# Kernel optimization log

Hardware: AMD Instinct MI355X
Metric: run time of the kernel (lower is better)

## Reference

```python
import jax, jax.numpy as jnp
import numpy as np

B, S, D, H = 2, 2048, 2048, 16
HD = D // H                     # head_dim = 128
ROTARY_BASE = 10000.0
CAP = 50.0                      # self.cap = FloatTensor([50.0])
FMIN = float(np.finfo(np.float32).min)
SCALE = 1.0 / np.sqrt(HD).astype(np.float32)


def _rope_sincos(seq_len, dim):
    # fixed_pos_embedding_factory with scaling_factor=1, no expand
    inv_freq = 1.0 / ROTARY_BASE ** (2.0 * jnp.arange(dim // 2, dtype=jnp.float32) / dim)
    pos = jnp.arange(seq_len, dtype=jnp.float32)
    ang = pos[:, None] * inv_freq[None, :]          # [S, dim/2]
    return jnp.sin(ang), jnp.cos(ang)


def _apply_rotary(x, sin, cos):
    # x: [B,S,H,hd]; sin/cos: [S,hd/2]. duplicate_interleave is a no-op
    # (view(-1,1).repeat(1,1).view(dim0,-1) returns m unchanged), so this is
    # NeoX-style (split-half) rotary.
    sin = sin[None, :, None, :]
    cos = cos[None, :, None, :]
    x1, x2 = jnp.split(x, 2, axis=-1)
    return jnp.concatenate([x1 * cos - x2 * sin, x2 * cos + x1 * sin], axis=-1)


def setup_inputs() -> dict:
    key = jax.random.key(0)
    kx, kq, kk, kv, ko = jax.random.split(key, 5)
    w = 0.02
    return {
        "x":  jax.random.normal(kx, (B, S, D), jnp.float32),
        "Wq": jax.random.normal(kq, (D, D), jnp.float32) * w,
        "Wk": jax.random.normal(kk, (D, D), jnp.float32) * w,
        "Wv": jax.random.normal(kv, (D, D), jnp.float32) * w,
        "Wo": jax.random.normal(ko, (D, D), jnp.float32) * w,
    }


def reference(x, Wq, Wk, Wv, Wo):
    # projections (bias=False)
    q = (x @ Wq).reshape(B, S, H, HD)
    k = (x @ Wk).reshape(B, S, H, HD)
    v = (x @ Wv).reshape(B, S, H, HD)

    # rotary over the full head dim (rotary_pct = 1.0)
    sin, cos = _rope_sincos(S, HD)
    q = _apply_rotary(q, sin, cos)
    k = _apply_rotary(k, sin, cos)

    # [B,H,S,hd]
    q = q.transpose(0, 2, 1, 3)
    k = k.transpose(0, 2, 1, 3)
    v = v.transpose(0, 2, 1, 3)

    # scores [B,H,S,S]
    scores = jnp.einsum("bhqd,bhkd->bhqk", q, k) * SCALE

    # logit cap: cap * tanh(x / cap)
    scores = CAP * jnp.tanh(scores / CAP)

    # causal mask (tril bias buffer), masked to finfo.min
    causal = jnp.tril(jnp.ones((S, S), dtype=bool))
    scores = jnp.where(causal[None, None], scores, FMIN)

    # LingvoSoftmax: softmax with an extra zero logit appended per row
    m = jnp.maximum(jnp.max(scores, axis=-1, keepdims=True), 0.0)
    e = jnp.exp(scores - m)
    denom = jnp.sum(e, axis=-1, keepdims=True) + jnp.exp(-m)
    probs = e / denom

    out = jnp.einsum("bhqk,bhkd->bhqd", probs, v)      # [B,H,S,hd]
    out = out.transpose(0, 2, 1, 3).reshape(B, S, D)
    return out @ Wo
```

## Files before the change

kernel.cpp:

```cpp
#include <hip/hip_runtime.h>
#include <hip/hip_bf16.h>

#define B_  2
#define S_  2048
#define D_  2048
#define H_  16
#define HD_ 128

typedef unsigned short u16;
typedef __attribute__((ext_vector_type(8))) short bf16x8;
typedef __attribute__((ext_vector_type(4))) float f32x4;
typedef __attribute__((ext_vector_type(16))) float f32x16;

#define GLOAD_LDS16(g, l)                                                     \
  __builtin_amdgcn_global_load_lds(                                           \
      (const __attribute__((address_space(1))) void*)(g),                     \
      (__attribute__((address_space(3))) void*)(l), 16, 0, 0)

__device__ __forceinline__ u16 f2bf(float f){
  unsigned u; __builtin_memcpy(&u, &f, 4);
  u += 0x7fffu + ((u >> 16) & 1u);
  return (u16)(u >> 16);
}
__device__ __forceinline__ float bf2f(u16 h){
  unsigned u = ((unsigned)h) << 16; float f; __builtin_memcpy(&f, &u, 4); return f;
}
__device__ __forceinline__ unsigned pack_bf16x2(float lo, float hi){
  __hip_bfloat162 h2 = __float22bfloat162_rn(float2{lo, hi});
  unsigned u; __builtin_memcpy(&u, &h2, 4); return u;
}

__global__ void cast_x_kernel(const float* __restrict__ x, u16* __restrict__ xb){
  int i = blockIdx.x * 256 + threadIdx.x;
  float4 v = reinterpret_cast<const float4*>(x)[i];
  ushort4 o; o.x = f2bf(v.x); o.y = f2bf(v.y); o.z = f2bf(v.z); o.w = f2bf(v.w);
  reinterpret_cast<ushort4*>(xb)[i] = o;
}

__global__ void wtrans_kernel(const float* __restrict__ w0, const float* __restrict__ w1,
                              const float* __restrict__ w2, const float* __restrict__ w3,
                              u16* __restrict__ o0, u16* __restrict__ o1,
                              u16* __restrict__ o2, u16* __restrict__ o3){
  __shared__ float t[32][33];
  const float* src; u16* dst;
  switch (blockIdx.z){
    case 0:  src = w0; dst = o0; break;
    case 1:  src = w1; dst = o1; break;
    case 2:  src = w2; dst = o2; break;
    default: src = w3; dst = o3; break;
  }
  int j0 = blockIdx.x * 32, i0 = blockIdx.y * 32;
  int tx = threadIdx.x & 31, ty = threadIdx.x >> 5;
  #pragma unroll
  for (int rr = 0; rr < 4; ++rr)
    t[ty + rr*8][tx] = src[(size_t)(i0 + ty + rr*8) * D_ + j0 + tx];
  __syncthreads();
  #pragma unroll
  for (int rr = 0; rr < 4; ++rr)
    dst[(size_t)(j0 + ty + rr*8) * D_ + i0 + tx] = f2bf(t[tx][ty + rr*8]);
}

template<int MODE>
__global__ __launch_bounds__(256) void gemm128_kernel(
    const u16* __restrict__ A,
    const u16* __restrict__ B0, const u16* __restrict__ B1, const u16* __restrict__ B2,
    u16* __restrict__ qb, u16* __restrict__ kb, u16* __restrict__ vtb,
    float* __restrict__ outp)
{
  constexpr int K = 2048;
  __shared__ u16 As[128 * 32];
  __shared__ u16 Bs[128 * 32];
  const int bid = blockIdx.x;
  const int xcd = bid & 7, loc = bid >> 3;
  const int mq  = loc & 31;
  const int nl  = loc >> 5;
  const int by  = (MODE == 0) ? (xcd * 6 + nl) : (xcd * 2 + nl);
  const int m0  = mq * 128;
  int which, n0;
  const u16* Bmat;
  if (MODE == 0){ which = by >> 4; n0 = (by & 15) * 128;
                  Bmat = (which == 0) ? B0 : ((which == 1) ? B1 : B2); }
  else          { which = 0; n0 = by * 128; Bmat = B0; }

  int tid  = threadIdx.x;
  int lane = tid & 63;
  int wid  = tid >> 6;
  int wr = wid >> 1, wc = wid & 1;
  int g = lane >> 4, r = lane & 15;

  f32x4 zero = {0.f, 0.f, 0.f, 0.f};
  f32x4 acc[4][4];
  #pragma unroll
  for (int i = 0; i < 4; ++i)
    #pragma unroll
    for (int j = 0; j < 4; ++j) acc[i][j] = zero;

  for (int kt = 0; kt < K; kt += 32){
    #pragma unroll
    for (int jj = 0; jj < 2; ++jj){
      int cbase = wid * 64 + jj * 256;
      int c  = cbase + lane;
      int rr = c >> 2, c8 = c & 3;
      GLOAD_LDS16(&A[(size_t)(m0 + rr) * K + kt + c8 * 8],    &As[cbase * 8]);
      GLOAD_LDS16(&Bmat[(size_t)(n0 + rr) * K + kt + c8 * 8], &Bs[cbase * 8]);
    }
    asm volatile("s_waitcnt vmcnt(0)" ::: "memory");
    __syncthreads();
    bf16x8 af[4], bfr[4];
    #pragma unroll
    for (int i = 0; i < 4; ++i)
      af[i]  = *reinterpret_cast<bf16x8*>(&As[(wr*64 + i*16 + r) * 32 + g * 8]);
    #pragma unroll
    for (int i = 0; i < 4; ++i)
      bfr[i] = *reinterpret_cast<bf16x8*>(&Bs[(wc*64 + i*16 + r) * 32 + g * 8]);
    #pragma unroll
    for (int i = 0; i < 4; ++i)
      #pragma unroll
      for (int j = 0; j < 4; ++j)
        acc[i][j] = __builtin_amdgcn_mfma_f32_16x16x32_bf16(af[i], bfr[j], acc[i][j], 0, 0, 0);
    __syncthreads();
  }

  #pragma unroll
  for (int i = 0; i < 4; ++i){
    int row0 = m0 + wr*64 + i*16 + g*4;
    int b  = row0 >> 11, s0 = row0 & (S_ - 1);
    #pragma unroll
    for (int j = 0; j < 4; ++j){
      int col = n0 + wc*64 + j*16 + r;
      if (MODE == 1){
        #pragma unroll
        for (int e = 0; e < 4; ++e)
          outp[(size_t)(row0 + e) * D_ + col] = acc[i][j][e];
      } else {
        int h = col >> 7, d = col & 127;
        int bh = b * H_ + h;
        if (which == 2){
          ushort4 pk;
          pk.x = f2bf(acc[i][j][0]); pk.y = f2bf(acc[i][j][1]);
          pk.z = f2bf(acc[i][j][2]); pk.w = f2bf(acc[i][j][3]);
          *reinterpret_cast<ushort4*>(&vtb[((size_t)bh * HD_ + d) * S_ + s0]) = pk;
        } else {
          u16* dstb = (which == 0) ? qb : kb;
          #pragma unroll
          for (int e = 0; e < 4; ++e)
            dstb[((size_t)bh * S_ + s0 + e) * HD_ + d] = f2bf(acc[i][j][e]);
        }
      }
    }
  }
}

__global__ void rope_kernel(u16* __restrict__ qbuf, u16* __restrict__ kbuf){
  int idx = blockIdx.x * 256 + threadIdx.x;
  int j  = idx & 63;
  int s  = (idx >> 6) & (S_ - 1);
  int bh = idx >> 17;
  const float LOG2_1E4 = 13.287712379549449f;
  float inv = exp2f(-(float)(2 * j) * (LOG2_1E4 / 128.f));
  float ang = (float)s * inv;
  float sn = __sinf(ang), cs = __cosf(ang);
  size_t base = ((size_t)bh * S_ + s) * HD_;
  float x1 = bf2f(qbuf[base + j]), x2 = bf2f(qbuf[base + 64 + j]);
  qbuf[base + j]      = f2bf(x1 * cs - x2 * sn);
  qbuf[base + 64 + j] = f2bf(x2 * cs + x1 * sn);
  float y1 = bf2f(kbuf[base + j]), y2 = bf2f(kbuf[base + 64 + j]);
  kbuf[base + j]      = f2bf(y1 * cs - y2 * sn);
  kbuf[base + 64 + j] = f2bf(y2 * cs + y1 * sn);
}

__global__ __launch_bounds__(256) void attn6_kernel(
  const u16* __restrict__ qbuf, const u16* __restrict__ kbuf,
  const u16* __restrict__ vtb,  u16* __restrict__ ob)
{
  __shared__ u16 Klds[2][64 * 128];
  __shared__ u16 Vlds[2][128 * 64];

  const int lane = threadIdx.x & 63;
  const int wid  = threadIdx.x >> 6;
  const int r    = lane & 31;
  const int hi   = lane >> 5;
  const int bh   = blockIdx.x;
  const int qblk = 15 - blockIdx.y;
  const int qc   = qblk * 128 + wid * 32;
  const int qc32 = qc >> 5;
  const int T    = 2 * qblk + 2;

  const float SCALE = 0.08838834764831845f;

  const size_t sbase = (size_t)bh * S_ * HD_;
  const size_t vbase = (size_t)bh * HD_ * S_;

  bf16x8 qf[8];
  {
    const u16* qrow = qbuf + sbase + (size_t)(qc + r) * HD_ + hi * 8;
    #pragma unroll
    for (int cc = 0; cc < 8; ++cc)
      qf[cc] = *reinterpret_cast<const bf16x8*>(qrow + cc * 16);
  }

  f32x16 oacc[4];
  #pragma unroll
  for (int i = 0; i < 4; ++i)
    #pragma unroll
    for (int j = 0; j < 16; ++j) oacc[i][j] = 0.f;
  float lsum = 0.f;

  auto stage = [&](int buf, int t){
    const int kv0 = t * 64;
    u16* Kt = &Klds[buf][0];
    u16* Vt = &Vlds[buf][0];
    #pragma unroll
    for (int j = 0; j < 4; ++j){
      const int cbase = j * 256 + wid * 64;
      const int ck = cbase + lane;
      const int krow = ck >> 4, kslot = ck & 15;
      GLOAD_LDS16(kbuf + sbase + (size_t)(kv0 + krow) * HD_ + ((kslot ^ (krow & 15)) * 8),
                  Kt + cbase * 8);
      const int vd = ck >> 3, vslot = ck & 7;
      GLOAD_LDS16(vtb + vbase + (size_t)vd * S_ + kv0 + ((vslot ^ (vd & 7)) * 8),
                  Vt + cbase * 8);
    }
  };

  stage(0, 0);
  asm volatile("s_waitcnt vmcnt(0)" ::: "memory");
  __syncthreads();

  for (int t = 0; t < T; ++t){
    const int cur = t & 1;
    if (t + 1 < T) stage(cur ^ 1, t + 1);

    const u16* Kt = &Klds[cur][0];
    const u16* Vt = &Vlds[cur][0];
    #pragma unroll
    for (int sub = 0; sub < 2; ++sub){
      const int t32 = 2 * t + sub;
      if (t32 <= qc32){
        const bool diag = (t32 == qc32);
        f32x16 sc;
        #pragma unroll
        for (int j = 0; j < 16; ++j) sc[j] = 0.f;
        #pragma unroll
        for (int cc = 0; cc < 8; ++cc){
          const int row = sub * 32 + r;
          const int slot = (cc * 2 + hi) ^ (r & 15);
          bf16x8 kf = *reinterpret_cast<const bf16x8*>(&Kt[row * 128 + slot * 8]);
          sc = __builtin_amdgcn_mfma_f32_32x32x16_bf16(kf, qf[cc], sc, 0, 0, 0);
        }
        float p[16];
        #pragma unroll
        for (int reg = 0; reg < 16; ++reg){
          float tt = sc[reg] * SCALE;
          float u  = tt * tt * 4.0e-4f;
          float capped = tt * (1.f - u * 0.33333333f + u * u * 0.13333333f);
          float pv = __expf(capped);
          if (diag){
            int kl = (reg & 3) + 8 * (reg >> 2) + 4 * hi;
            if (kl > r) pv = 0.f;
          }
          p[reg] = pv;
          lsum += pv;
        }
        unsigned a[4], b[4];
        #pragma unroll
        for (int r4 = 0; r4 < 4; ++r4){
          a[r4] = pack_bf16x2(p[r4*4+0], p[r4*4+1]);
          b[r4] = pack_bf16x2(p[r4*4+2], p[r4*4+3]);
        }
        unsigned ra0 = __shfl_xor(hi ? a[0] : a[1], 32);
        unsigned rb0 = __shfl_xor(hi ? b[0] : b[1], 32);
        unsigned ra1 = __shfl_xor(hi ? a[2] : a[3], 32);
        unsigned rb1 = __shfl_xor(hi ? b[2] : b[3], 32);
        unsigned pw[8];
        pw[0] = hi ? ra0 : a[0];  pw[1] = hi ? rb0 : b[0];
        pw[2] = hi ? a[1] : ra0;  pw[3] = hi ? b[1] : rb0;
        pw[4] = hi ? ra1 : a[2];  pw[5] = hi ? rb1 : b[2];
        pw[6] = hi ? a[3] : ra1;  pw[7] = hi ? b[3] : rb1;
        bf16x8 pb0, pb1;
        __builtin_memcpy(&pb0, &pw[0], 16);
        __builtin_memcpy(&pb1, &pw[4], 16);
        #pragma unroll
        for (int i = 0; i < 4; ++i){
          const int d  = i * 32 + r;
          const int sw = d & 7;
          bf16x8 vf0 = *reinterpret_cast<const bf16x8*>(
              &Vt[d * 64 + (((sub * 4 + hi) ^ sw) * 8)]);
          oacc[i] = __builtin_amdgcn_mfma_f32_32x32x16_bf16(vf0, pb0, oacc[i], 0, 0, 0);
          bf16x8 vf1 = *reinterpret_cast<const bf16x8*>(
              &Vt[d * 64 + (((sub * 4 + 2 + hi) ^ sw) * 8)]);
          oacc[i] = __builtin_amdgcn_mfma_f32_32x32x16_bf16(vf1, pb1, oacc[i], 0, 0, 0);
        }
      }
    }
    asm volatile("s_waitcnt vmcnt(0)" ::: "memory");
    __syncthreads();
  }

  float lt = lsum + __shfl_xor(lsum, 32);
  float linv = 1.0f / (1.0f + lt);

  const int b = bh >> 4, h = bh & 15;
  u16* orow = ob + ((size_t)(b * S_ + qc + r)) * D_ + h * HD_;
  #pragma unroll
  for (int i = 0; i < 4; ++i){
    #pragma unroll
    for (int r4 = 0; r4 < 4; ++r4){
      ushort4 st;
      st.x = f2bf(oacc[i][r4*4+0] * linv);
      st.y = f2bf(oacc[i][r4*4+1] * linv);
      st.z = f2bf(oacc[i][r4*4+2] * linv);
      st.w = f2bf(oacc[i][r4*4+3] * linv);
      *reinterpret_cast<ushort4*>(orow + i*32 + r4*8 + hi*4) = st;
    }
  }
}

extern "C" void kernel_launch(void* const* d_in, const int* in_sizes, int n_in,
                              void* d_out, int out_size, void* d_ws, size_t ws_size,
                              hipStream_t stream){
  const float* x  = (const float*)d_in[0];
  const float* Wq = (const float*)d_in[1];
  const float* Wk = (const float*)d_in[2];
  const float* Wv = (const float*)d_in[3];
  const float* Wo = (const float*)d_in[4];
  float* out = (float*)d_out;
  char* ws = (char*)d_ws;

  u16* xb   = (u16*)(ws);
  u16* wtq  = (u16*)(ws + (size_t)(16u << 20));
  u16* wtk  = (u16*)(ws + (size_t)(24u << 20));
  u16* wtv  = (u16*)(ws + (size_t)(32u << 20));
  u16* wto  = (u16*)(ws + (size_t)(40u << 20));
  u16* qbuf = (u16*)(ws + (size_t)(48u << 20));
  u16* kbuf = (u16*)(ws + (size_t)(64u << 20));
  u16* vtb  = (u16*)(ws + (size_t)(80u << 20));
  u16* atb  = (u16*)(ws + (size_t)(96u << 20));

  cast_x_kernel<<<8192, 256, 0, stream>>>(x, xb);
  wtrans_kernel<<<dim3(64, 64, 4), 256, 0, stream>>>(Wq, Wk, Wv, Wo, wtq, wtk, wtv, wto);
  gemm128_kernel<0><<<1536, 256, 0, stream>>>(xb, wtq, wtk, wtv,
                                              qbuf, kbuf, vtb, nullptr);
  rope_kernel<<<16384, 256, 0, stream>>>(qbuf, kbuf);
  attn6_kernel<<<dim3(32, 16), 256, 0, stream>>>(qbuf, kbuf, vtb, atb);
  gemm128_kernel<1><<<512, 256, 0, stream>>>(atb, wto, nullptr, nullptr,
                                             nullptr, nullptr, nullptr, out);
}
```

Baseline: 292.3 us.

## Deepen GEMM K-tile to 64 with XOR-swizzled LDS and fold attention constants into exp2

The projection GEMM now stages 64-wide K tiles instead of 32 and applies an XOR swizzle on the 16-byte slots, both at global-to-LDS load time and at fragment read time. This halves the number of barrier/wait iterations and is meant to avoid LDS bank conflicts. The grid changes from a 1D XCD-aware mapping to a plain 2D grid, which gives up the explicit L2 locality per XCD. In attention, the scale, the tanh-cap polynomial and log2(e) are folded into constants so softmax uses fmaf plus a native exp2, cutting ALU work per score.

```diff
diff --git a/kernel.cpp b/kernel.cpp
--- a/kernel.cpp
+++ b/kernel.cpp
@@ -68,14 +68,10 @@
     float* __restrict__ outp)
 {
   constexpr int K = 2048;
-  __shared__ u16 As[128 * 32];
-  __shared__ u16 Bs[128 * 32];
-  const int bid = blockIdx.x;
-  const int xcd = bid & 7, loc = bid >> 3;
-  const int mq  = loc & 31;
-  const int nl  = loc >> 5;
-  const int by  = (MODE == 0) ? (xcd * 6 + nl) : (xcd * 2 + nl);
-  const int m0  = mq * 128;
+  __shared__ u16 As[128 * 64];
+  __shared__ u16 Bs[128 * 64];
+  int m0 = blockIdx.x * 128;
+  int by = blockIdx.y;
   int which, n0;
   const u16* Bmat;
   if (MODE == 0){ which = by >> 4; n0 = (by & 15) * 128;
@@ -87,6 +83,7 @@
   int wid  = tid >> 6;
   int wr = wid >> 1, wc = wid & 1;
   int g = lane >> 4, r = lane & 15;
+  const int sx = r & 7;
 
   f32x4 zero = {0.f, 0.f, 0.f, 0.f};
   f32x4 acc[4][4];
@@ -95,29 +92,36 @@
     #pragma unroll
     for (int j = 0; j < 4; ++j) acc[i][j] = zero;
 
-  for (int kt = 0; kt < K; kt += 32){
-    #pragma unroll
-    for (int jj = 0; jj < 2; ++jj){
-      int cbase = wid * 64 + jj * 256;
+  for (int kt = 0; kt < K; kt += 64){
+    #pragma unroll
+    for (int j = 0; j < 4; ++j){
+      int cbase = j * 256 + wid * 64;
       int c  = cbase + lane;
-      int rr = c >> 2, c8 = c & 3;
-      GLOAD_LDS16(&A[(size_t)(m0 + rr) * K + kt + c8 * 8],    &As[cbase * 8]);
-      GLOAD_LDS16(&Bmat[(size_t)(n0 + rr) * K + kt + c8 * 8], &Bs[cbase * 8]);
+      int row = c >> 3, sl = c & 7;
+      GLOAD_LDS16(&A[(size_t)(m0 + row) * K + kt + ((sl ^ (row & 7)) * 8)],
+                  &As[cbase * 8]);
+      GLOAD_LDS16(&Bmat[(size_t)(n0 + row) * K + kt + ((sl ^ (row & 7)) * 8)],
+                  &Bs[cbase * 8]);
     }
     asm volatile("s_waitcnt vmcnt(0)" ::: "memory");
     __syncthreads();
-    bf16x8 af[4], bfr[4];
-    #pragma unroll
-    for (int i = 0; i < 4; ++i)
-      af[i]  = *reinterpret_cast<bf16x8*>(&As[(wr*64 + i*16 + r) * 32 + g * 8]);
-    #pragma unroll
-    for (int i = 0; i < 4; ++i)
-      bfr[i] = *reinterpret_cast<bf16x8*>(&Bs[(wc*64 + i*16 + r) * 32 + g * 8]);
-    #pragma unroll
-    for (int i = 0; i < 4; ++i)
+    #pragma unroll
+    for (int kk = 0; kk < 2; ++kk){
+      bf16x8 af[4], bfr[4];
       #pragma unroll
-      for (int j = 0; j < 4; ++j)
-        acc[i][j] = __builtin_amdgcn_mfma_f32_16x16x32_bf16(af[i], bfr[j], acc[i][j], 0, 0, 0);
+      for (int i = 0; i < 4; ++i)
+        af[i]  = *reinterpret_cast<bf16x8*>(
+            &As[(wr*64 + i*16 + r) * 64 + (((kk*4 + g) ^ sx) * 8)]);
+      #pragma unroll
+      for (int i = 0; i < 4; ++i)
+        bfr[i] = *reinterpret_cast<bf16x8*>(
+            &Bs[(wc*64 + i*16 + r) * 64 + (((kk*4 + g) ^ sx) * 8)]);
+      #pragma unroll
+      for (int i = 0; i < 4; ++i)
+        #pragma unroll
+        for (int j = 0; j < 4; ++j)
+          acc[i][j] = __builtin_amdgcn_mfma_f32_16x16x32_bf16(af[i], bfr[j], acc[i][j], 0, 0, 0);
+    }
     __syncthreads();
   }
 
@@ -186,7 +190,8 @@
   const int qc32 = qc >> 5;
   const int T    = 2 * qblk + 2;
 
-  const float SCALE = 0.08838834764831845f;
+  const float C1 = 0.12751757f;
+  const float C2 = 1.9218114e-4f;
 
   const size_t sbase = (size_t)bh * S_ * HD_;
   const size_t vbase = (size_t)bh * HD_ * S_;
@@ -251,10 +256,11 @@
         float p[16];
         #pragma unroll
         for (int reg = 0; reg < 16; ++reg){
-          float tt = sc[reg] * SCALE;
-          float u  = tt * tt * 4.0e-4f;
-          float capped = tt * (1.f - u * 0.33333333f + u * u * 0.13333333f);
-          float pv = __expf(capped);
+          float tt2 = sc[reg] * C1;
+          float w   = tt2 * tt2 * C2;
+          float qp  = fmaf(w, 0.13333333f, -0.33333333f);
+          float y   = fmaf(tt2 * w, qp, tt2);
+          float pv  = __builtin_amdgcn_exp2f(y);
           if (diag){
             int kl = (reg & 3) + 8 * (reg >> 2) + 4 * hi;
             if (kl > r) pv = 0.f;
@@ -339,10 +345,10 @@
 
   cast_x_kernel<<<8192, 256, 0, stream>>>(x, xb);
   wtrans_kernel<<<dim3(64, 64, 4), 256, 0, stream>>>(Wq, Wk, Wv, Wo, wtq, wtk, wtv, wto);
-  gemm128_kernel<0><<<1536, 256, 0, stream>>>(xb, wtq, wtk, wtv,
-                                              qbuf, kbuf, vtb, nullptr);
+  gemm128_kernel<0><<<dim3(32, 48), 256, 0, stream>>>(xb, wtq, wtk, wtv,
+                                                      qbuf, kbuf, vtb, nullptr);
   rope_kernel<<<16384, 256, 0, stream>>>(qbuf, kbuf);
   attn6_kernel<<<dim3(32, 16), 256, 0, stream>>>(qbuf, kbuf, vtb, atb);
-  gemm128_kernel<1><<<512, 256, 0, stream>>>(atb, wto, nullptr, nullptr,
-                                             nullptr, nullptr, nullptr, out);
-}
+  gemm128_kernel<1><<<dim3(32, 16), 256, 0, stream>>>(atb, wto, nullptr, nullptr,
+                                                      nullptr, nullptr, nullptr, out);
+}
```

After: 274.7 us. 1.06x faster.
